# Kernel tuning notes

Measured on AMD Instinct MI355X. Metric: run time of the kernel, lower is better.

The kernel has to match this reference:

```python
import jax, jax.numpy as jnp
import numpy as np

D_MODEL, D_MLP, D_HEAD, N_HEADS, SEQ, BATCH = 1024, 4096, 64, 16, 2048, 2


def setup_inputs() -> dict:
    key = jax.random.key(0)
    ks = jax.random.split(key, 7)
    s = 1.0 / np.sqrt(D_MODEL)
    return {
        "x": jax.random.normal(ks[0], (BATCH, SEQ, D_MODEL), jnp.float32),
        "W_K": jax.random.normal(ks[1], (N_HEADS, D_HEAD, D_MODEL), jnp.float32) * s,
        "W_Q": jax.random.normal(ks[2], (N_HEADS, D_HEAD, D_MODEL), jnp.float32) * s,
        "W_V": jax.random.normal(ks[3], (N_HEADS, D_HEAD, D_MODEL), jnp.float32) * s,
        "W_O": jax.random.normal(ks[4], (D_MODEL, N_HEADS * D_HEAD), jnp.float32) * s,
        "W_in": jax.random.normal(ks[5], (D_MLP, D_MODEL), jnp.float32) * s,
        "b_in": jnp.zeros((D_MLP,), jnp.float32),
        "W_out": jax.random.normal(ks[6], (D_MODEL, D_MLP), jnp.float32) * s,
        "b_out": jnp.zeros((D_MODEL,), jnp.float32),
    }


def _block(x, W_K, W_Q, W_V, W_O, W_in, b_in, W_out, b_out):
    S = x.shape[-2]
    # attention
    k = jnp.einsum('ihd,bpd->biph', W_K, x)
    q = jnp.einsum('ihd,bpd->biph', W_Q, x)
    v = jnp.einsum('ihd,bpd->biph', W_V, x)
    scores = jnp.einsum('biph,biqh->biqp', k, q)  # [B,H,S(query q),S(key p)]
    causal = jnp.tril(jnp.ones((S, S), x.dtype))
    masked = jnp.tril(scores) - 1e10 * (1.0 - causal)
    attn = jax.nn.softmax(masked / np.sqrt(D_HEAD), axis=-1)
    z = jnp.einsum('biph,biqp->biqh', v, attn)  # [B,H,S,d_head]
    z_flat = jnp.transpose(z, (0, 2, 1, 3)).reshape(x.shape[0], S, -1)  # b q (i h)
    attn_out = jnp.einsum('df,bqf->bqd', W_O, z_flat)
    x = x + attn_out
    # MLP
    h = jax.nn.relu(jnp.einsum('md,bpd->bpm', W_in, x) + b_in)
    x = x + jnp.einsum('dm,bpm->bpd', W_out, h) + b_out
    return x


def reference(x, W_K, W_Q, W_V, W_O, W_in, b_in, W_out, b_out):
    return _block(x, W_K, W_Q, W_V, W_O, W_in, b_in, W_out, b_out)
```

## Files before the change

kernel.cpp:

```cpp
#include <hip/hip_runtime.h>

typedef unsigned short u16;
typedef __bf16 bf16x8 __attribute__((ext_vector_type(8)));
typedef float f32x4 __attribute__((ext_vector_type(4)));
typedef u16 u16x8 __attribute__((ext_vector_type(8), may_alias));
typedef u16 u16x4 __attribute__((ext_vector_type(4), may_alias));
typedef unsigned int u32x4 __attribute__((ext_vector_type(4)));

#define D_MODEL 1024
#define D_MLP   4096
#define D_HEAD  64
#define N_HEADS 16
#define SEQ     2048
#define BATCH   2
#define BS      (BATCH * SEQ)
#define QKV_N   3072
#define QSCALE  0.18033688011112042f

__device__ __forceinline__ u16 f2b(float f) {
  unsigned u = __builtin_bit_cast(unsigned, f);
  u += 0x7fffu + ((u >> 16) & 1u);
  return (u16)(u >> 16);
}

__device__ __forceinline__ unsigned cvtpk_bf16(float lo, float hi) {
  unsigned r;
  asm("v_cvt_pk_bf16_f32 %0, %1, %2" : "=v"(r) : "v"(lo), "v"(hi));
  return r;
}

__device__ __forceinline__ void gload_lds16(const u16* g, u16* l) {
  __builtin_amdgcn_global_load_lds(
      (const __attribute__((address_space(1))) unsigned int*)g,
      (__attribute__((address_space(3))) unsigned int*)l, 16, 0, 0);
}

__global__ __launch_bounds__(256) void cvt_all(
    const float* __restrict__ x,  const float* __restrict__ wq,
    const float* __restrict__ wk, const float* __restrict__ wv,
    const float* __restrict__ wo, const float* __restrict__ wi,
    const float* __restrict__ wu,
    u16* __restrict__ xb, u16* __restrict__ wqkv, u16* __restrict__ wo_b,
    u16* __restrict__ win_b, u16* __restrict__ wout_b)
{
  const int i = blockIdx.x * 256 + threadIdx.x;
  const float* src; u16* dst; int j;
  if (i < 1048576)      { src = x;  dst = xb;              j = i; }
  else if (i < 1310720) { src = wq; dst = wqkv;            j = i - 1048576; }
  else if (i < 1572864) { src = wk; dst = wqkv + 1048576;  j = i - 1310720; }
  else if (i < 1835008) { src = wv; dst = wqkv + 2097152;  j = i - 1572864; }
  else if (i < 2097152) { src = wo; dst = wo_b;            j = i - 1835008; }
  else if (i < 3145728) { src = wi; dst = win_b;           j = i - 2097152; }
  else                  { src = wu; dst = wout_b;          j = i - 3145728; }
  float4 v = ((const float4*)src)[j];
  u16x4 o;
  o[0] = f2b(v.x); o[1] = f2b(v.y); o[2] = f2b(v.z); o[3] = f2b(v.w);
  ((u16x4*)dst)[j] = o;
}

template<int MODE, int BM>
__global__ __launch_bounds__(256) void gemm_bt(
    const u16* __restrict__ A, const u16* __restrict__ Bw,
    int M, int N, int K,
    u16* __restrict__ outb, float* __restrict__ outf,
    const float* __restrict__ resid, const float* __restrict__ bias,
    u16* __restrict__ vtp, int gx)
{
  constexpr int MI = BM / 32;
  __shared__ u16 Asm_[BM * 64];
  __shared__ u16 Bsm_[128 * 64];
  const int t = threadIdx.x;
  const int lane = t & 63;
  const int l15 = lane & 15, l4 = lane >> 4;
  const int w = t >> 6;
  const int wr = w >> 1, wc = w & 1;

  int bx, by;
  if constexpr (BM == 64) {
    bx = blockIdx.x & 7;
    by = blockIdx.x >> 3;
  } else {
    const int xcd = blockIdx.x & 7;
    const int local = blockIdx.x >> 3;
    const int rw = gx >> 2;
    const int rx = xcd & 3, ry = xcd >> 2;
    const int c = local >> 4, r0 = local & 15;
    bx = rx * rw + c;
    by = ry * 16 + r0;
  }
  int z = 0;
  if (MODE == 3) { z = bx >> 3; bx &= 7; }
  const int m0 = by * BM;
  const int n0 = bx * 128;
  const int kb = (MODE == 3) ? z * (K >> 2) : 0;
  const int ke = (MODE == 3) ? kb + (K >> 2) : K;

  f32x4 acc[MI][4] = {};

  for (int k0 = kb; k0 < ke; k0 += 64) {
    __syncthreads();
#pragma unroll
    for (int i = 0; i < 4; ++i) {
      int s = i * 256 + t;
      int row = s >> 3;
      int sl = s & 7;
      int gc = ((sl ^ (row & 7)) << 3);
      const u16* gb = Bw + (size_t)(n0 + row) * K + (k0 + gc);
      u16* lb = Bsm_ + (i * 256 + (t & ~63)) * 8;
      if (BM == 128 || i < 2) {
        const u16* ga = A + (size_t)(m0 + row) * K + (k0 + gc);
        u16* la = Asm_ + (i * 256 + (t & ~63)) * 8;
        gload_lds16(ga, la);
      }
      gload_lds16(gb, lb);
    }
    asm volatile("s_waitcnt vmcnt(0)" ::: "memory");
    __syncthreads();
#pragma unroll
    for (int kk = 0; kk < 2; ++kk) {
      bf16x8 af[MI], bfr[4];
#pragma unroll
      for (int mi = 0; mi < MI; ++mi) {
        int row = wr * (BM / 2) + mi * 16 + l15;
        int sl2 = (kk * 4 + l4) ^ (row & 7);
        u16x8 ua = *(const u16x8*)(Asm_ + row * 64 + sl2 * 8);
        af[mi] = __builtin_bit_cast(bf16x8, ua);
      }
#pragma unroll
      for (int ni = 0; ni < 4; ++ni) {
        int row = wc * 64 + ni * 16 + l15;
        int sl2 = (kk * 4 + l4) ^ (row & 7);
        u16x8 ub = *(const u16x8*)(Bsm_ + row * 64 + sl2 * 8);
        bfr[ni] = __builtin_bit_cast(bf16x8, ub);
      }
#pragma unroll
      for (int mi = 0; mi < MI; ++mi)
#pragma unroll
        for (int ni = 0; ni < 4; ++ni)
          acc[mi][ni] = __builtin_amdgcn_mfma_f32_16x16x32_bf16(af[mi], bfr[ni], acc[mi][ni], 0, 0, 0);
    }
  }

#pragma unroll
  for (int mi = 0; mi < MI; ++mi) {
    int rowb = m0 + wr * (BM / 2) + mi * 16 + l4 * 4;
#pragma unroll
    for (int ni = 0; ni < 4; ++ni) {
      int col = n0 + wc * 64 + ni * 16 + l15;
#pragma unroll
      for (int r = 0; r < 4; ++r) {
        float v = acc[mi][ni][r];
        int row = rowb + r;
        if (MODE == 0) {
          if (col < 2048) {
            float o = (col < 1024) ? v * QSCALE : v;
            outb[((size_t)row << 11) + col] = f2b(o);
          } else {
            int c2 = col - 2048;
            size_t vi = (((size_t)((row >> 11) * 1024 + c2)) << 11) + (row & (SEQ - 1));
            vtp[vi] = f2b(v);
          }
        } else if (MODE == 3) {
          outf[(size_t)z * M * N + (size_t)row * N + col] = v;
        } else {
          size_t idx = (size_t)row * N + col;
          if (MODE == 1) {
            float o = v + resid[idx];
            outf[idx] = o;
            outb[idx] = f2b(o);
          } else {
            float o = v + bias[col];
            o = o > 0.f ? o : 0.f;
            outb[idx] = f2b(o);
          }
        }
      }
    }
  }
}

__global__ __launch_bounds__(256) void reduce4_kernel(const float* __restrict__ part,
                                                      const float* __restrict__ resid,
                                                      const float* __restrict__ bias,
                                                      float* __restrict__ out) {
  const int i = blockIdx.x * 256 + threadIdx.x;
  const size_t S = (size_t)BS * D_MODEL;
  float4 a = ((const float4*)part)[i];
  float4 b = ((const float4*)(part + S))[i];
  float4 c = ((const float4*)(part + 2 * S))[i];
  float4 d = ((const float4*)(part + 3 * S))[i];
  float4 r = ((const float4*)resid)[i];
  float4 bi = ((const float4*)bias)[i & 255];
  float4 o;
  o.x = a.x + b.x + c.x + d.x + r.x + bi.x;
  o.y = a.y + b.y + c.y + d.y + r.y + bi.y;
  o.z = a.z + b.z + c.z + d.z + r.z + bi.z;
  o.w = a.w + b.w + c.w + d.w + r.w + bi.w;
  ((float4*)out)[i] = o;
}

__global__ __launch_bounds__(256) void attn_kernel(const u16* __restrict__ qk,
                                                   const u16* __restrict__ vT,
                                                   u16* __restrict__ zb)
{
  __shared__ u16 Kl[2][128 * 64];
  __shared__ u16 Vl[2][64 * 136];
  const int t = threadIdx.x;
  const int w = t >> 6;
  const int lane = t & 63;
  const int l15 = lane & 15, l4 = lane >> 4;
  const int blk = blockIdx.x;
  const int bh = blk & 31;
  const int qb = 15 - (blk >> 5);
  const int b = bh >> 4, h = bh & 15;
  const int q0w = qb * 128 + w * 32;
  const int ttmax = qb;

  bf16x8 qf[2][2];
#pragma unroll
  for (int s = 0; s < 2; ++s) {
    const u16* qp = qk + (((size_t)(b * SEQ + q0w + s * 16 + l15)) << 11) + h * 64 + l4 * 8;
    qf[s][0] = __builtin_bit_cast(bf16x8, *(const u16x8*)(qp));
    qf[s][1] = __builtin_bit_cast(bf16x8, *(const u16x8*)(qp + 32));
  }

  const int srow = t >> 3;
  const int sgc = ((t & 7) ^ (srow & 7)) * 8;
  const u16* kgbase = qk + (((size_t)(b * SEQ + srow)) << 11) + 1024 + h * 64 + sgc;
  u16* kldst = &Kl[0][0] + (t & ~63) * 8;
  const int vd2 = t >> 2, q4 = t & 3;
  const u16* vgbase = vT + (((size_t)(bh * 64 + vd2)) << 11);

  f32x4 zacc[2][4] = {};
  float m_run[2] = {-1e30f, -1e30f}, l_run[2] = {0.f, 0.f};

  auto stageK = [&](int buf, int tt) {
    const u16* kg = kgbase + ((size_t)tt << 18);
    u16* kld = kldst + buf * (128 * 64);
#pragma unroll
    for (int i = 0; i < 4; ++i)
      gload_lds16(kg + ((size_t)i << 16), kld + i * 2048);
  };

  auto compute = [&](int buf, int tt) {
    const bool last = (tt == ttmax);
#pragma unroll
    for (int s = 0; s < 2; ++s) {
      f32x4 sf[8] = {};
      __builtin_amdgcn_s_setprio(1);
#pragma unroll
      for (int ks = 0; ks < 8; ++ks) {
        const int row = ks * 16 + l15;
#pragma unroll
        for (int kc = 0; kc < 2; ++kc) {
          const int slot = (kc * 4 + l4) ^ (row & 7);
          bf16x8 kf = __builtin_bit_cast(bf16x8,
              *(const u16x8*)&Kl[buf][row * 64 + slot * 8]);
          sf[ks] = __builtin_amdgcn_mfma_f32_16x16x32_bf16(kf, qf[s][kc], sf[ks], 0, 0, 0);
        }
      }
      __builtin_amdgcn_s_setprio(0);

      if (last) {
        const int qq = q0w + s * 16 + l15;
        const int pb = tt * 128 + l4 * 4;
#pragma unroll
        for (int ks = 0; ks < 8; ++ks)
#pragma unroll
          for (int r = 0; r < 4; ++r)
            sf[ks][r] = (pb + ks * 16 + r <= qq) ? sf[ks][r] : -1e30f;
      }

      float mk[8];
#pragma unroll
      for (int ks = 0; ks < 8; ++ks)
        mk[ks] = fmaxf(fmaxf(sf[ks][0], sf[ks][1]), fmaxf(sf[ks][2], sf[ks][3]));
      float mt = fmaxf(fmaxf(fmaxf(mk[0], mk[1]), fmaxf(mk[2], mk[3])),
                       fmaxf(fmaxf(mk[4], mk[5]), fmaxf(mk[6], mk[7])));
      mt = fmaxf(mt, __shfl_xor(mt, 16));
      mt = fmaxf(mt, __shfl_xor(mt, 32));
      const float mn = fmaxf(m_run[s], mt);
      const float sc = __builtin_amdgcn_exp2f(m_run[s] - mn);
      m_run[s] = mn;
      float pv[8][4];
      float rs = 0.f;
#pragma unroll
      for (int ks = 0; ks < 8; ++ks)
#pragma unroll
        for (int r = 0; r < 4; ++r) {
          pv[ks][r] = __builtin_amdgcn_exp2f(sf[ks][r] - mn);
          rs += pv[ks][r];
        }
      rs += __shfl_xor(rs, 16);
      rs += __shfl_xor(rs, 32);
      l_run[s] = l_run[s] * sc + rs;

#pragma unroll
      for (int dn = 0; dn < 4; ++dn)
#pragma unroll
        for (int r = 0; r < 4; ++r) zacc[s][dn][r] *= sc;

      __builtin_amdgcn_s_setprio(1);
#pragma unroll
      for (int g = 0; g < 4; ++g) {
        u32x4 pu;
        pu[0] = cvtpk_bf16(pv[2 * g][0], pv[2 * g][1]);
        pu[1] = cvtpk_bf16(pv[2 * g][2], pv[2 * g][3]);
        pu[2] = cvtpk_bf16(pv[2 * g + 1][0], pv[2 * g + 1][1]);
        pu[3] = cvtpk_bf16(pv[2 * g + 1][2], pv[2 * g + 1][3]);
        const bf16x8 pa = __builtin_bit_cast(bf16x8, pu);
#pragma unroll
        for (int dn = 0; dn < 4; ++dn) {
          bf16x8 vfr = __builtin_bit_cast(bf16x8,
              *(const u16x8*)&Vl[buf][(dn * 16 + l15) * 136 + g * 32 + l4 * 8]);
          zacc[s][dn] = __builtin_amdgcn_mfma_f32_16x16x32_bf16(vfr, pa, zacc[s][dn], 0, 0, 0);
        }
      }
      __builtin_amdgcn_s_setprio(0);
    }
  };

  stageK(0, 0);
  {
#pragma unroll
    for (int g = 0; g < 4; ++g) {
      const u16* vg = vgbase + g * 32 + q4 * 4;
      u16x4 lo = *(const u16x4*)(vg);
      u16x4 hi = *(const u16x4*)(vg + 16);
      *(u16x8*)&Vl[0][vd2 * 136 + g * 32 + q4 * 8] =
          __builtin_shufflevector(lo, hi, 0, 1, 2, 3, 4, 5, 6, 7);
    }
  }
  asm volatile("s_waitcnt vmcnt(0)" ::: "memory");
  __syncthreads();

  int cur = 0;
  for (int tt = 0; tt <= ttmax; ++tt) {
    const bool more = tt < ttmax;
    u16x4 lo[4], hi[4];
    if (more) {
      stageK(cur ^ 1, tt + 1);
#pragma unroll
      for (int g = 0; g < 4; ++g) {
        const u16* vg = vgbase + (tt + 1) * 128 + g * 32 + q4 * 4;
        lo[g] = *(const u16x4*)(vg);
        hi[g] = *(const u16x4*)(vg + 16);
      }
    }
    compute(cur, tt);
    if (more) {
#pragma unroll
      for (int g = 0; g < 4; ++g)
        *(u16x8*)&Vl[cur ^ 1][vd2 * 136 + g * 32 + q4 * 8] =
            __builtin_shufflevector(lo[g], hi[g], 0, 1, 2, 3, 4, 5, 6, 7);
    }
    asm volatile("s_waitcnt vmcnt(0)" ::: "memory");
    __syncthreads();
    cur ^= 1;
  }

#pragma unroll
  for (int s = 0; s < 2; ++s) {
    const float inv = 1.f / l_run[s];
    const size_t rowoff = ((size_t)(b * SEQ + q0w + s * 16 + l15)) * D_MODEL + h * 64 + l4 * 4;
#pragma unroll
    for (int dn = 0; dn < 4; ++dn) {
      u16x4 o;
#pragma unroll
      for (int r = 0; r < 4; ++r) o[r] = f2b(zacc[s][dn][r] * inv);
      *(u16x4*)(zb + rowoff + dn * 16) = o;
    }
  }
}

extern "C" void kernel_launch(void* const* d_in, const int* in_sizes, int n_in,
                              void* d_out, int out_size, void* d_ws, size_t ws_size,
                              hipStream_t stream) {
  const float* x     = (const float*)d_in[0];
  const float* W_K   = (const float*)d_in[1];
  const float* W_Q   = (const float*)d_in[2];
  const float* W_V   = (const float*)d_in[3];
  const float* W_O   = (const float*)d_in[4];
  const float* W_in  = (const float*)d_in[5];
  const float* b_in  = (const float*)d_in[6];
  const float* W_out = (const float*)d_in[7];
  const float* b_out = (const float*)d_in[8];
  float* out = (float*)d_out;

  char* p = (char*)d_ws;
  float* x1f  = (float*)p;         p += (size_t)BS * D_MODEL * 4;
  u16* hb     = (u16*)p;           p += (size_t)BS * D_MLP * 2;
  u16* wout_b = (u16*)p;           p += (size_t)D_MODEL * D_MLP * 2;
  u16* xb     = (u16*)p;           p += (size_t)BS * D_MODEL * 2;
  u16* wqkv   = (u16*)p;           p += (size_t)QKV_N * D_MODEL * 2;
  u16* wo_b   = (u16*)p;           p += (size_t)D_MODEL * D_MODEL * 2;
  u16* win_b  = (u16*)p;           p += (size_t)D_MLP * D_MODEL * 2;
  u16* qk     = (u16*)p;           p += (size_t)BS * 2048 * 2;
  u16* vt     = (u16*)p;           p += (size_t)BATCH * 1024 * SEQ * 2;
  u16* zb     = (u16*)p;           p += (size_t)BS * D_MODEL * 2;
  u16* x1b    = (u16*)p;           p += (size_t)BS * D_MODEL * 2;
  float* part = (float*)xb;

  cvt_all<<<dim3(16384), 256, 0, stream>>>(
      x, W_Q, W_K, W_V, W_O, W_in, W_out, xb, wqkv, wo_b, win_b, wout_b);

  gemm_bt<0, 128><<<dim3(24 * 32), 256, 0, stream>>>(
      xb, wqkv, BS, QKV_N, D_MODEL, qk, nullptr, nullptr, nullptr, vt, 24);

  attn_kernel<<<dim3(512), 256, 0, stream>>>(qk, vt, zb);

  gemm_bt<1, 64><<<dim3(512), 256, 0, stream>>>(
      zb, wo_b, BS, D_MODEL, D_MODEL, x1b, x1f, x, nullptr, nullptr, 8);

  gemm_bt<2, 128><<<dim3(32 * 32), 256, 0, stream>>>(
      x1b, win_b, BS, D_MLP, D_MODEL, hb, nullptr, nullptr, b_in, nullptr, 32);

  gemm_bt<3, 128><<<dim3(32 * 32), 256, 0, stream>>>(
      hb, wout_b, BS, D_MODEL, D_MLP, nullptr, part, nullptr, nullptr, nullptr, 32);

  reduce4_kernel<<<dim3(BS * D_MODEL / 4 / 256), 256, 0, stream>>>(part, x1f, b_out, out);
}
```

Before: 252.2 us.

## Halve MLP-out split-K and batch attention QK/PV MFMAs across both query sub-tiles

The MLP down-projection split-K goes from 4 to 2 K-slices, which halves the partial buffers written and read by the reduction kernel but leaves half as many blocks (512) to occupy the GPU. The attention compute loop is restructured so the QK^T MFMAs for both 16-row query sub-tiles share each K fragment load, and the PV MFMAs for both sub-tiles share each V fragment load. This cuts LDS reads and interleaves independent MFMA chains, at the cost of higher register pressure from holding two score tiles at once.

After: 237.5 us (median of 4 runs). -5.8%, faster.

```diff
diff --git a/kernel.cpp b/kernel.cpp
--- a/kernel.cpp
+++ b/kernel.cpp
@@ -92,8 +92,8 @@
   if (MODE == 3) { z = bx >> 3; bx &= 7; }
   const int m0 = by * BM;
   const int n0 = bx * 128;
-  const int kb = (MODE == 3) ? z * (K >> 2) : 0;
-  const int ke = (MODE == 3) ? kb + (K >> 2) : K;
+  const int kb = (MODE == 3) ? z * (K >> 1) : 0;
+  const int ke = (MODE == 3) ? kb + (K >> 1) : K;
 
   f32x4 acc[MI][4] = {};
 
@@ -179,23 +179,20 @@
   }
 }
 
-__global__ __launch_bounds__(256) void reduce4_kernel(const float* __restrict__ part,
+__global__ __launch_bounds__(256) void reduce2_kernel(const float* __restrict__ part,
                                                       const float* __restrict__ resid,
                                                       const float* __restrict__ bias,
                                                       float* __restrict__ out) {
   const int i = blockIdx.x * 256 + threadIdx.x;
-  const size_t S = (size_t)BS * D_MODEL;
   float4 a = ((const float4*)part)[i];
-  float4 b = ((const float4*)(part + S))[i];
-  float4 c = ((const float4*)(part + 2 * S))[i];
-  float4 d = ((const float4*)(part + 3 * S))[i];
+  float4 b = ((const float4*)(part + (size_t)BS * D_MODEL))[i];
   float4 r = ((const float4*)resid)[i];
   float4 bi = ((const float4*)bias)[i & 255];
   float4 o;
-  o.x = a.x + b.x + c.x + d.x + r.x + bi.x;
-  o.y = a.y + b.y + c.y + d.y + r.y + bi.y;
-  o.z = a.z + b.z + c.z + d.z + r.z + bi.z;
-  o.w = a.w + b.w + c.w + d.w + r.w + bi.w;
+  o.x = a.x + b.x + r.x + bi.x;
+  o.y = a.y + b.y + r.y + bi.y;
+  o.z = a.z + b.z + r.z + bi.z;
+  o.w = a.w + b.w + r.w + bi.w;
   ((float4*)out)[i] = o;
 }
 
@@ -244,80 +241,93 @@
 
   auto compute = [&](int buf, int tt) {
     const bool last = (tt == ttmax);
+    f32x4 sf[2][8] = {};
+    __builtin_amdgcn_s_setprio(1);
+#pragma unroll
+    for (int ks = 0; ks < 8; ++ks) {
+      const int row = ks * 16 + l15;
+#pragma unroll
+      for (int kc = 0; kc < 2; ++kc) {
+        const int slot = (kc * 4 + l4) ^ (row & 7);
+        bf16x8 kf = __builtin_bit_cast(bf16x8,
+            *(const u16x8*)&Kl[buf][row * 64 + slot * 8]);
+        sf[0][ks] = __builtin_amdgcn_mfma_f32_16x16x32_bf16(kf, qf[0][kc], sf[0][ks], 0, 0, 0);
+        sf[1][ks] = __builtin_amdgcn_mfma_f32_16x16x32_bf16(kf, qf[1][kc], sf[1][ks], 0, 0, 0);
+      }
+    }
+    __builtin_amdgcn_s_setprio(0);
+
+    if (last) {
+      const int pb = tt * 128 + l4 * 4;
+#pragma unroll
+      for (int s = 0; s < 2; ++s) {
+        const int qq = q0w + s * 16 + l15;
+#pragma unroll
+        for (int ks = 0; ks < 8; ++ks)
+#pragma unroll
+          for (int r = 0; r < 4; ++r)
+            sf[s][ks][r] = (pb + ks * 16 + r <= qq) ? sf[s][ks][r] : -1e30f;
+      }
+    }
+
+    float mn[2], sc_[2];
 #pragma unroll
     for (int s = 0; s < 2; ++s) {
-      f32x4 sf[8] = {};
-      __builtin_amdgcn_s_setprio(1);
-#pragma unroll
-      for (int ks = 0; ks < 8; ++ks) {
-        const int row = ks * 16 + l15;
-#pragma unroll
-        for (int kc = 0; kc < 2; ++kc) {
-          const int slot = (kc * 4 + l4) ^ (row & 7);
-          bf16x8 kf = __builtin_bit_cast(bf16x8,
-              *(const u16x8*)&Kl[buf][row * 64 + slot * 8]);
-          sf[ks] = __builtin_amdgcn_mfma_f32_16x16x32_bf16(kf, qf[s][kc], sf[ks], 0, 0, 0);
-        }
-      }
-      __builtin_amdgcn_s_setprio(0);
-
-      if (last) {
-        const int qq = q0w + s * 16 + l15;
-        const int pb = tt * 128 + l4 * 4;
-#pragma unroll
-        for (int ks = 0; ks < 8; ++ks)
-#pragma unroll
-          for (int r = 0; r < 4; ++r)
-            sf[ks][r] = (pb + ks * 16 + r <= qq) ? sf[ks][r] : -1e30f;
-      }
-
       float mk[8];
 #pragma unroll
       for (int ks = 0; ks < 8; ++ks)
-        mk[ks] = fmaxf(fmaxf(sf[ks][0], sf[ks][1]), fmaxf(sf[ks][2], sf[ks][3]));
+        mk[ks] = fmaxf(fmaxf(sf[s][ks][0], sf[s][ks][1]), fmaxf(sf[s][ks][2], sf[s][ks][3]));
       float mt = fmaxf(fmaxf(fmaxf(mk[0], mk[1]), fmaxf(mk[2], mk[3])),
                        fmaxf(fmaxf(mk[4], mk[5]), fmaxf(mk[6], mk[7])));
       mt = fmaxf(mt, __shfl_xor(mt, 16));
       mt = fmaxf(mt, __shfl_xor(mt, 32));
-      const float mn = fmaxf(m_run[s], mt);
-      const float sc = __builtin_amdgcn_exp2f(m_run[s] - mn);
-      m_run[s] = mn;
-      float pv[8][4];
+      mn[s] = fmaxf(m_run[s], mt);
+      sc_[s] = __builtin_amdgcn_exp2f(m_run[s] - mn[s]);
+      m_run[s] = mn[s];
+    }
+#pragma unroll
+    for (int s = 0; s < 2; ++s) {
       float rs = 0.f;
 #pragma unroll
       for (int ks = 0; ks < 8; ++ks)
 #pragma unroll
         for (int r = 0; r < 4; ++r) {
-          pv[ks][r] = __builtin_amdgcn_exp2f(sf[ks][r] - mn);
-          rs += pv[ks][r];
+          sf[s][ks][r] = __builtin_amdgcn_exp2f(sf[s][ks][r] - mn[s]);
+          rs += sf[s][ks][r];
         }
       rs += __shfl_xor(rs, 16);
       rs += __shfl_xor(rs, 32);
-      l_run[s] = l_run[s] * sc + rs;
-
+      l_run[s] = l_run[s] * sc_[s] + rs;
 #pragma unroll
       for (int dn = 0; dn < 4; ++dn)
 #pragma unroll
-        for (int r = 0; r < 4; ++r) zacc[s][dn][r] *= sc;
-
-      __builtin_amdgcn_s_setprio(1);
+        for (int r = 0; r < 4; ++r) zacc[s][dn][r] *= sc_[s];
+    }
+
+    bf16x8 pa[2][4];
+#pragma unroll
+    for (int s = 0; s < 2; ++s)
 #pragma unroll
       for (int g = 0; g < 4; ++g) {
         u32x4 pu;
-        pu[0] = cvtpk_bf16(pv[2 * g][0], pv[2 * g][1]);
-        pu[1] = cvtpk_bf16(pv[2 * g][2], pv[2 * g][3]);
-        pu[2] = cvtpk_bf16(pv[2 * g + 1][0], pv[2 * g + 1][1]);
-        pu[3] = cvtpk_bf16(pv[2 * g + 1][2], pv[2 * g + 1][3]);
-        const bf16x8 pa = __builtin_bit_cast(bf16x8, pu);
-#pragma unroll
-        for (int dn = 0; dn < 4; ++dn) {
-          bf16x8 vfr = __builtin_bit_cast(bf16x8,
-              *(const u16x8*)&Vl[buf][(dn * 16 + l15) * 136 + g * 32 + l4 * 8]);
-          zacc[s][dn] = __builtin_amdgcn_mfma_f32_16x16x32_bf16(vfr, pa, zacc[s][dn], 0, 0, 0);
-        }
-      }
-      __builtin_amdgcn_s_setprio(0);
-    }
+        pu[0] = cvtpk_bf16(sf[s][2 * g][0], sf[s][2 * g][1]);
+        pu[1] = cvtpk_bf16(sf[s][2 * g][2], sf[s][2 * g][3]);
+        pu[2] = cvtpk_bf16(sf[s][2 * g + 1][0], sf[s][2 * g + 1][1]);
+        pu[3] = cvtpk_bf16(sf[s][2 * g + 1][2], sf[s][2 * g + 1][3]);
+        pa[s][g] = __builtin_bit_cast(bf16x8, pu);
+      }
+
+    __builtin_amdgcn_s_setprio(1);
+#pragma unroll
+    for (int g = 0; g < 4; ++g)
+#pragma unroll
+      for (int dn = 0; dn < 4; ++dn) {
+        bf16x8 vfr = __builtin_bit_cast(bf16x8,
+            *(const u16x8*)&Vl[buf][(dn * 16 + l15) * 136 + g * 32 + l4 * 8]);
+        zacc[0][dn] = __builtin_amdgcn_mfma_f32_16x16x32_bf16(vfr, pa[0][g], zacc[0][dn], 0, 0, 0);
+        zacc[1][dn] = __builtin_amdgcn_mfma_f32_16x16x32_bf16(vfr, pa[1][g], zacc[1][dn], 0, 0, 0);
+      }
+    __builtin_amdgcn_s_setprio(0);
   };
 
   stageK(0, 0);
@@ -415,8 +425,8 @@
   gemm_bt<2, 128><<<dim3(32 * 32), 256, 0, stream>>>(
       x1b, win_b, BS, D_MLP, D_MODEL, hb, nullptr, nullptr, b_in, nullptr, 32);
 
-  gemm_bt<3, 128><<<dim3(32 * 32), 256, 0, stream>>>(
-      hb, wout_b, BS, D_MODEL, D_MLP, nullptr, part, nullptr, nullptr, nullptr, 32);
-
-  reduce4_kernel<<<dim3(BS * D_MODEL / 4 / 256), 256, 0, stream>>>(part, x1f, b_out, out);
-}
+  gemm_bt<3, 128><<<dim3(16 * 32), 256, 0, stream>>>(
+      hb, wout_b, BS, D_MODEL, D_MLP, nullptr, part, nullptr, nullptr, nullptr, 16);
+
+  reduce2_kernel<<<dim3(BS * D_MODEL / 4 / 256), 256, 0, stream>>>(part, x1f, b_out, out);
+}
```
